# Performance work log

Measured on AMD Instinct MI355X. Metric: run time of the kernel, lower is better.

Reference implementation:

```python
import jax, jax.numpy as jnp
import numpy as np
import math

N, E, G = 16000, 128000, 64
D, H, O, L, HID = 64, 4, 64, 5, 128
EPS = 1e-5

def _ln(x, g, b):
    mu = x.mean(-1, keepdims=True)
    var = ((x - mu) ** 2).mean(-1, keepdims=True)
    return (x - mu) / jnp.sqrt(var + EPS) * g + b

def _softplus_b64(x):
    # torch nn.Softplus(beta=64, threshold=64): x if 64*x > 64 else log1p(exp(64*x))/64
    z = jnp.minimum(x * 64.0, 64.0)
    return jnp.where(x * 64.0 > 64.0, x, jnp.log1p(jnp.exp(z)) / 64.0)

def setup_inputs() -> dict:
    key = jax.random.key(0)
    ks = jax.random.split(key, 32)
    s = 0.05
    d = {
        'x': jax.random.normal(ks[0], (N, 4), jnp.float32),
        'edge_attr': jax.random.normal(ks[1], (E, 9), jnp.float32),
        'edge_index': jax.random.randint(ks[2], (2, E), 0, N),
        'batch': jnp.sort(jax.random.randint(ks[3], (N,), 0, G)),
        'W_atom': jax.random.normal(ks[4], (4, D)) * s, 'b_atom': jnp.zeros((D,)),
        'We1': jax.random.normal(ks[5], (9, D)) * s, 'be1': jnp.zeros((D,)),
        'We2': jax.random.normal(ks[6], (D, D)) * s, 'be2': jnp.zeros((D,)),
        'Wq': jax.random.normal(ks[7], (L, D, H * O)) * s, 'bq': jnp.zeros((L, H * O)),
        'Wk': jax.random.normal(ks[8], (L, D, H * O)) * s, 'bk': jnp.zeros((L, H * O)),
        'Wv': jax.random.normal(ks[9], (L, D, H * O)) * s, 'bv': jnp.zeros((L, H * O)),
        'Wedge': jax.random.normal(ks[10], (L, D, H * O)) * s, 'bedge': jnp.zeros((L, H * O)),
        'Wfea': jax.random.normal(ks[11], (L, D, O)) * s, 'bfea': jnp.zeros((L, O)),
        'Wcat': jax.random.normal(ks[12], (L, H * O, O)) * s, 'bcat': jnp.zeros((L, O)),
        'Wupd': jax.random.normal(ks[13], (L, 3 * O, 3 * O)) * s, 'bupd': jnp.zeros((L, 3 * O)),
        'Wmsg': jax.random.normal(ks[14], (L, 3 * O, O)) * s, 'bmsg': jnp.zeros((L, O)),
        'g_msg': jnp.ones((L, O)), 'be_msg': jnp.zeros((L, O)),
        'g_ln': jnp.ones((L, 3 * O)), 'be_ln': jnp.zeros((L, 3 * O)),
        'g_bn': jnp.ones((L, O)), 'be_bn': jnp.zeros((L, O)),
        'Wfc': jax.random.normal(ks[15], (D, HID)) * s, 'bfc': jnp.zeros((HID,)),
        'Wout': jax.random.normal(ks[16], (HID, 1)) * s, 'bout': jnp.zeros((1,)),
    }
    return d

def _forward(x, edge_attr, W_atom, b_atom, We1, be1, We2, be2, Wq, bq, Wk, bk, Wv, bv,
             Wedge, bedge, Wfea, bfea, Wcat, bcat, Wupd, bupd, Wmsg, bmsg,
             g_msg, be_msg, g_ln, be_ln, g_bn, be_bn, Wfc, bfc, Wout, bout,
             edge_index, batch):
    src, dst = edge_index[0], edge_index[1]  # x_j = src, x_i = dst (flow source_to_target)
    h = x @ W_atom + b_atom  # [N, D]
    e = _softplus_b64(edge_attr @ We1 + be1) @ We2 + be2  # [E, D]
    scale = 1.0 / math.sqrt(3.0 * O)
    for l in range(L):
        Q = (h @ Wq[l] + bq[l]).reshape(N, H, O)
        K = (h @ Wk[l] + bk[l]).reshape(N, H, O)
        V = (h @ Wv[l] + bv[l]).reshape(N, H, O)
        Eh = (e @ Wedge[l] + bedge[l]).reshape(E, H, O)
        Qi = Q[dst]
        q_ij = jnp.concatenate([Qi, Qi, Qi], axis=-1)                 # [E, H, 3O]
        k_ij = jnp.concatenate([K[dst], K[src], Eh], axis=-1)
        v_ij = jnp.concatenate([V[dst], V[src], Eh], axis=-1)
        alpha = q_ij * k_ij * scale
        gate = jax.nn.sigmoid(_ln(alpha, g_ln[l], be_ln[l]))
        m = gate * (v_ij @ Wupd[l] + bupd[l])
        m = _ln(m @ Wmsg[l] + bmsg[l], g_msg[l], be_msg[l])           # [E, H, O]
        agg = jax.ops.segment_sum(m, dst, num_segments=N).reshape(N, H * O)
        out = agg @ Wcat[l] + bcat[l]
        mu = out.mean(0)
        var = ((out - mu) ** 2).mean(0)  # biased var, BN training mode
        out = (out - mu) / jnp.sqrt(var + EPS) * g_bn[l] + be_bn[l]
        h = jax.nn.silu(out) + (h @ Wfea[l] + bfea[l])
    ones = jnp.ones((N,), h.dtype)
    cnt = jax.ops.segment_sum(ones, batch, num_segments=G)
    pooled = jax.ops.segment_sum(h, batch, num_segments=G) / jnp.maximum(cnt, 1.0)[:, None]
    z = jax.nn.silu(pooled @ Wfc + bfc)
    return z @ Wout + bout  # [G, 1]

def reference(x, edge_attr, edge_index, batch, W_atom, b_atom, We1, be1, We2, be2,
              Wq, bq, Wk, bk, Wv, bv, Wedge, bedge, Wfea, bfea, Wcat, bcat,
              Wupd, bupd, Wmsg, bmsg, g_msg, be_msg, g_ln, be_ln, g_bn, be_bn,
              Wfc, bfc, Wout, bout):
    return _forward(x, edge_attr, W_atom, b_atom, We1, be1, We2, be2, Wq, bq, Wk, bk,
                    Wv, bv, Wedge, bedge, Wfea, bfea, Wcat, bcat, Wupd, bupd,
                    Wmsg, bmsg, g_msg, be_msg, g_ln, be_ln, g_bn, be_bn,
                    Wfc, bfc, Wout, bout, edge_index, batch)
```

## Files before the change

kernel.cpp:

```cpp
#include <hip/hip_runtime.h>
#include <hip/hip_bf16.h>
#include <math.h>

#define N_NODES 16000
#define N_EDGES 128000
#define N_GRAPH 64
#define NL 5
#define EPSV 1e-5f
#define SCALE 0.07216878364870323f

#define PC 2048
#define ECOLS 1024
#define TILE 16
#define SCR 260

typedef __hip_bfloat16 bf16;
typedef __attribute__((ext_vector_type(8))) short short8;
typedef __attribute__((ext_vector_type(4))) short s4v;
typedef __attribute__((ext_vector_type(4))) float f32x4;
union S8U { short8 v; s4v h[2]; };

__device__ __forceinline__ ushort f2b(float x) {
    union { float f; uint u; } v; v.f = x;
    uint r = v.u + 0x7fffu + ((v.u >> 16) & 1u);
    return (ushort)(r >> 16);
}
__device__ __forceinline__ float b2fu(ushort u) { union { uint u; float f; } v; v.u = (uint)u << 16; return v.f; }

__global__ void pack_w(const float* __restrict__ Wq, const float* __restrict__ Wk,
                       const float* __restrict__ Wv, const float* __restrict__ Wupd,
                       const float* __restrict__ Wedge,
                       short* __restrict__ Wnp, short* __restrict__ Wep) {
    int idx = blockIdx.x * 256 + threadIdx.x;
    int total = NL * 64 * (PC + ECOLS);
    if (idx >= total) return;
    int c = idx % (PC + ECOLS);
    int k = (idx / (PC + ECOLS)) % 64;
    int l = idx / (64 * (PC + ECOLS));
    if (c < PC) {
        float v = 0.f;
        if (c < 256) v = Wq[(l*64 + k)*256 + c];
        else if (c < 512) v = Wk[(l*64 + k)*256 + (c - 256)];
        else if (c < 1280) {
            int cc = c - 512, hd = cc / 192, p = cc % 192;
            float s = 0.f;
            for (int q = 0; q < 64; ++q)
                s += Wv[(l*64 + k)*256 + hd*64 + q] * Wupd[(l*192 + q)*192 + p];
            v = s;
        } else {
            int cc = c - 1280, hd = cc / 192, p = cc % 192;
            float s = 0.f;
            for (int q = 0; q < 64; ++q)
                s += Wv[(l*64 + k)*256 + hd*64 + q] * Wupd[(l*192 + 64 + q)*192 + p];
            v = s;
        }
        int t = c >> 4, s = k >> 5, lane = (c & 15) | (((k & 31) >> 3) << 4), jj = k & 7;
        size_t fo = ((size_t)(t*2 + s)*64 + lane)*8 + jj;
        ushort hi = f2b(v);
        ushort lo = f2b(v - b2fu(hi));
        Wnp[(size_t)l*2*64*PC + fo] = (short)hi;
        Wnp[(size_t)l*2*64*PC + (size_t)64*PC + fo] = (short)lo;
    } else {
        int ce = c - PC;
        float v;
        if (ce < 256) v = Wedge[(l*64 + k)*256 + ce];
        else {
            int cc = ce - 256, hd = cc / 192, p = cc % 192;
            float s = 0.f;
            for (int q = 0; q < 64; ++q)
                s += Wedge[(l*64 + k)*256 + hd*64 + q] * Wupd[(l*192 + 128 + q)*192 + p];
            v = s;
        }
        int t = ce >> 4, s = k >> 5, lane = (ce & 15) | (((k & 31) >> 3) << 4), jj = k & 7;
        size_t fo = ((size_t)(t*2 + s)*64 + lane)*8 + jj;
        ushort hi = f2b(v);
        ushort lo = f2b(v - b2fu(hi));
        Wep[(size_t)l*2*64*ECOLS + fo] = (short)hi;
        Wep[(size_t)l*2*64*ECOLS + (size_t)64*ECOLS + fo] = (short)lo;
    }
}

__global__ void pack_wmsg(const float* __restrict__ Wmsg, short* __restrict__ Wmf) {
    int idx = blockIdx.x * 256 + threadIdx.x;
    if (idx >= NL*192*64) return;
    int col = idx & 63, k = (idx >> 6) % 192, l = idx / (192*64);
    float v = Wmsg[(size_t)(l*192 + k)*64 + col];
    int t = col >> 4, s = k >> 5, lane = (col & 15) | (((k & 31) >> 3) << 4), j = k & 7;
    Wmf[(size_t)l*12288 + ((size_t)((t*6 + s)*64) + lane)*8 + j] = (short)f2b(v);
}

__global__ void pack_b(const float* __restrict__ bq, const float* __restrict__ bk,
                       const float* __restrict__ bv, const float* __restrict__ Wupd,
                       const float* __restrict__ bupd, const float* __restrict__ bedge,
                       float* __restrict__ bnp, float* __restrict__ bep) {
    int idx = blockIdx.x * 256 + threadIdx.x;
    int total = NL * (PC + ECOLS);
    if (idx >= total) return;
    int c = idx % (PC + ECOLS);
    int l = idx / (PC + ECOLS);
    if (c < PC) {
        float v = 0.f;
        if (c < 256) v = bq[l*256 + c];
        else if (c < 512) v = bk[l*256 + c - 256];
        else if (c < 1280) {
            int cc = c - 512, hd = cc / 192, p = cc % 192;
            float s = 0.f;
            for (int k = 0; k < 64; ++k) s += bv[l*256 + hd*64 + k] * Wupd[(l*192 + k)*192 + p];
            v = s;
        } else {
            int cc = c - 1280, hd = cc / 192, p = cc % 192;
            float s = 0.f;
            for (int k = 0; k < 64; ++k) s += bv[l*256 + hd*64 + k] * Wupd[(l*192 + 64 + k)*192 + p];
            v = s;
        }
        bnp[l*PC + c] = v;
    } else {
        int ce = c - PC;
        float v;
        if (ce < 256) v = bedge[l*256 + ce];
        else {
            int cc = ce - 256, hd = cc / 192, p = cc % 192;
            float s = bupd[l*192 + p];
            for (int k = 0; k < 64; ++k) s += bedge[l*256 + hd*64 + k] * Wupd[(l*192 + 128 + k)*192 + p];
            v = s;
        }
        bep[l*ECOLS + ce] = v;
    }
}

__global__ void hist_k(const int* __restrict__ ei, int* __restrict__ hist) {
    int e = blockIdx.x * 256 + threadIdx.x;
    if (e < N_EDGES) atomicAdd(&hist[ei[N_EDGES + e]], 1);
}

__global__ void scan_k(const int* __restrict__ hist, int* __restrict__ binCur) {
    __shared__ int sBuf[256];
    __shared__ int sCarry;
    int tid = threadIdx.x;
    if (tid == 0) sCarry = 0;
    __syncthreads();
    for (int base = 0; base < N_NODES; base += 256) {
        int v = (base + tid < N_NODES) ? hist[base + tid] : 0;
        sBuf[tid] = v; __syncthreads();
        #pragma unroll
        for (int ofs = 1; ofs < 256; ofs <<= 1) {
            int t = (tid >= ofs) ? sBuf[tid - ofs] : 0;
            __syncthreads();
            sBuf[tid] += t;
            __syncthreads();
        }
        if (base + tid < N_NODES) binCur[base + tid] = sCarry + sBuf[tid] - v;
        __syncthreads();
        if (tid == 0) sCarry += sBuf[255];
        __syncthreads();
    }
}

__global__ void scatter_k(const int* __restrict__ ei, int* __restrict__ binCur,
                          int* __restrict__ perm, int* __restrict__ srcs, int* __restrict__ dsts) {
    int e = blockIdx.x * 256 + threadIdx.x;
    if (e < N_EDGES) {
        int d = ei[N_EDGES + e];
        int pos = atomicAdd(&binCur[d], 1);
        perm[pos] = e;
        srcs[pos] = ei[e];
        dsts[pos] = d;
    }
}

__global__ void init_h(const float* __restrict__ x, const float* __restrict__ W_atom,
                       const float* __restrict__ b_atom, float* __restrict__ h) {
    int idx = blockIdx.x * 256 + threadIdx.x;
    int d = idx & 63, n = idx >> 6;
    float s = b_atom[d];
    #pragma unroll
    for (int j = 0; j < 4; ++j) s += x[n*4 + j] * W_atom[j*64 + d];
    h[idx] = s;
}

__global__ void init_e(const float* __restrict__ ea, const float* __restrict__ We1,
                       const float* __restrict__ be1, const float* __restrict__ We2,
                       const float* __restrict__ be2, float* __restrict__ ef) {
    __shared__ float sT[4][64];
    int tid = threadIdx.x, d = tid & 63, sub = tid >> 6;
    int e = blockIdx.x * 4 + sub;
    float s = be1[d];
    #pragma unroll
    for (int j = 0; j < 9; ++j) s += ea[e*9 + j] * We1[j*64 + d];
    float x64 = s * 64.f;
    float sp = (x64 > 64.f) ? s : log1pf(__expf(fminf(x64, 64.f))) * (1.f/64.f);
    sT[sub][d] = sp;
    float acc = be2[d];
    #pragma unroll
    for (int k = 0; k < 64; ++k) acc += sT[sub][k] * We2[k*64 + d];
    ef[(size_t)e*64 + d] = acc;
}

#define CPAD 260
__global__ __launch_bounds__(256, 8) void proj_mfma(
    const float* __restrict__ A, const short* __restrict__ Whi, const short* __restrict__ Wlo,
    const float* __restrict__ bias, ushort* __restrict__ out, int M) {
    __shared__ short aHi[2*64*8];
    __shared__ short aLo[2*64*8];
    __shared__ ushort cTile[16*CPAD];
    int tid = threadIdx.x;
    int row0 = blockIdx.y * 16;
    int col0 = blockIdx.x * 256;
    {
        int r = tid >> 4, k0 = (tid & 15) * 4;
        const float4 v = *(const float4*)(A + (size_t)(row0 + r)*64 + k0);
        int s = k0 >> 5, lane = r | (((k0 & 31) >> 3) << 4), j0 = k0 & 7;
        ushort4 hb, lb;
        hb.x = f2b(v.x); lb.x = f2b(v.x - b2fu(hb.x));
        hb.y = f2b(v.y); lb.y = f2b(v.y - b2fu(hb.y));
        hb.z = f2b(v.z); lb.z = f2b(v.z - b2fu(hb.z));
        hb.w = f2b(v.w); lb.w = f2b(v.w - b2fu(hb.w));
        *(ushort4*)&aHi[(s*64 + lane)*8 + j0] = hb;
        *(ushort4*)&aLo[(s*64 + lane)*8 + j0] = lb;
    }
    __syncthreads();
    int w = tid >> 6, lane = tid & 63;
    short8 a0h = *(const short8*)&aHi[(0*64 + lane)*8];
    short8 a1h = *(const short8*)&aHi[(1*64 + lane)*8];
    short8 a0l = *(const short8*)&aLo[(0*64 + lane)*8];
    short8 a1l = *(const short8*)&aLo[(1*64 + lane)*8];
    int cl = lane & 15, rg = lane >> 4;
    #pragma unroll
    for (int nt = 0; nt < 4; ++nt) {
        int t = (col0 >> 4) + w*4 + nt;
        const short* bph = Whi + ((size_t)(t*2)*64 + lane)*8;
        const short* bpl = Wlo + ((size_t)(t*2)*64 + lane)*8;
        short8 b0h = *(const short8*)bph;
        short8 b1h = *(const short8*)(bph + 64*8);
        short8 b0l = *(const short8*)bpl;
        short8 b1l = *(const short8*)(bpl + 64*8);
        f32x4 acc = {0.f, 0.f, 0.f, 0.f};
        acc = __builtin_amdgcn_mfma_f32_16x16x32_bf16(a0h, b0h, acc, 0, 0, 0);
        acc = __builtin_amdgcn_mfma_f32_16x16x32_bf16(a1h, b1h, acc, 0, 0, 0);
        acc = __builtin_amdgcn_mfma_f32_16x16x32_bf16(a0l, b0h, acc, 0, 0, 0);
        acc = __builtin_amdgcn_mfma_f32_16x16x32_bf16(a1l, b1h, acc, 0, 0, 0);
        acc = __builtin_amdgcn_mfma_f32_16x16x32_bf16(a0h, b0l, acc, 0, 0, 0);
        acc = __builtin_amdgcn_mfma_f32_16x16x32_bf16(a1h, b1l, acc, 0, 0, 0);
        int ccol = w*64 + nt*16 + cl;
        float bv = bias[col0 + ccol];
        #pragma unroll
        for (int r = 0; r < 4; ++r)
            cTile[(rg*4 + r)*CPAD + ccol] = f2b(acc[r] + bv);
    }
    __syncthreads();
    {
        int r = tid >> 4, cs = (tid & 15) * 16;
        ushort* dst = out + (size_t)(row0 + r)*M + col0 + cs;
        const ushort* srcp = &cTile[r*CPAD + cs];
        #pragma unroll
        for (int q = 0; q < 4; ++q)
            *(ushort4*)(dst + q*4) = *(const ushort4*)(srcp + q*4);
    }
}

__global__ __launch_bounds__(256) void hf_proj(const float* __restrict__ h,
                                               const float* __restrict__ Wfea,
                                               const float* __restrict__ bfea,
                                               float* __restrict__ HF) {
    __shared__ float sW[64*64];
    __shared__ __align__(16) float sA[4][64];
    int tid = threadIdx.x;
    for (int i = tid; i < 4096; i += 256) sW[i] = Wfea[i];
    int c = tid & 63, no = tid >> 6;
    int n0 = blockIdx.x * 4;
    sA[no][c] = h[(size_t)(n0 + no)*64 + c];
    __syncthreads();
    float acc = bfea[c];
    #pragma unroll
    for (int k4 = 0; k4 < 16; ++k4) {
        float4 av = *(const float4*)&sA[no][k4*4];
        acc += av.x*sW[(k4*4+0)*64+c] + av.y*sW[(k4*4+1)*64+c]
             + av.z*sW[(k4*4+2)*64+c] + av.w*sW[(k4*4+3)*64+c];
    }
    HF[(size_t)(n0 + no)*64 + c] = acc;
}

__global__ __launch_bounds__(256, 4) void edge_fused(
    const bf16* __restrict__ P, const float* __restrict__ ef,
    const short* __restrict__ Wef, const float* __restrict__ bef,
    const int* __restrict__ perm, const int* __restrict__ srcs, const int* __restrict__ dsts,
    const short* __restrict__ Wmf, const float* __restrict__ bmsg,
    const float* __restrict__ g_ln, const float* __restrict__ be_ln,
    const float* __restrict__ g_msg, const float* __restrict__ be_msg,
    float* __restrict__ agg) {
    __shared__ short aHi[2*64*8];
    __shared__ short aLo[2*64*8];
    __shared__ __align__(16) ushort scr[4][TILE][SCR];
    int tid = threadIdx.x, lane = tid & 63, hd = tid >> 6;
    int e0 = blockIdx.x * TILE;
    {
        int r = tid >> 4, k0 = (tid & 15) * 4;
        int ep = perm[e0 + r];
        const float4 v = *(const float4*)(ef + (size_t)ep*64 + k0);
        int s = k0 >> 5, alane = r | (((k0 & 31) >> 3) << 4), j0 = k0 & 7;
        ushort4 hb, lb;
        hb.x = f2b(v.x); lb.x = f2b(v.x - b2fu(hb.x));
        hb.y = f2b(v.y); lb.y = f2b(v.y - b2fu(hb.y));
        hb.z = f2b(v.z); lb.z = f2b(v.z - b2fu(hb.z));
        hb.w = f2b(v.w); lb.w = f2b(v.w - b2fu(hb.w));
        *(ushort4*)&aHi[(s*64 + alane)*8 + j0] = hb;
        *(ushort4*)&aLo[(s*64 + alane)*8 + j0] = lb;
    }
    __syncthreads();
    int cl = lane & 15, rg = lane >> 4;
    {
        short8 a0h = *(const short8*)&aHi[(0*64 + lane)*8];
        short8 a1h = *(const short8*)&aHi[(1*64 + lane)*8];
        short8 a0l = *(const short8*)&aLo[(0*64 + lane)*8];
        short8 a1l = *(const short8*)&aLo[(1*64 + lane)*8];
        #pragma unroll
        for (int tt = 0; tt < 16; ++tt) {
            int tg = (tt < 4) ? (hd*4 + tt) : (16 + hd*12 + (tt - 4));
            const short* bph = Wef + ((size_t)(tg*2)*64 + lane)*8;
            const short* bpl = bph + (size_t)64*ECOLS;
            short8 b0h = *(const short8*)bph;
            short8 b1h = *(const short8*)(bph + 512);
            short8 b0l = *(const short8*)bpl;
            short8 b1l = *(const short8*)(bpl + 512);
            float bv = bef[tg*16 + cl];
            f32x4 acc = {bv, bv, bv, bv};
            acc = __builtin_amdgcn_mfma_f32_16x16x32_bf16(a0h, b0h, acc, 0, 0, 0);
            acc = __builtin_amdgcn_mfma_f32_16x16x32_bf16(a1h, b1h, acc, 0, 0, 0);
            acc = __builtin_amdgcn_mfma_f32_16x16x32_bf16(a0l, b0h, acc, 0, 0, 0);
            acc = __builtin_amdgcn_mfma_f32_16x16x32_bf16(a1l, b1h, acc, 0, 0, 0);
            acc = __builtin_amdgcn_mfma_f32_16x16x32_bf16(a0h, b0l, acc, 0, 0, 0);
            acc = __builtin_amdgcn_mfma_f32_16x16x32_bf16(a1h, b1l, acc, 0, 0, 0);
            int wcol = (tt < 4) ? (tt*16 + cl) : (64 + (tt - 4)*16 + cl);
            #pragma unroll
            for (int r = 0; r < 4; ++r)
                scr[hd][rg*4 + r][wcol] = f2b(acc[r]);
        }
    }
    float gl0 = g_ln[lane], gl1 = g_ln[64 + lane], gl2 = g_ln[128 + lane];
    float bl0 = be_ln[lane], bl1 = be_ln[64 + lane], bl2 = be_ln[128 + lane];
    #pragma unroll 2
    for (int it = 0; it < TILE; ++it) {
        int src = srcs[e0 + it], dst = dsts[e0 + it];
        const bf16* Pd = P + (size_t)dst * PC;
        const bf16* Ps = P + (size_t)src * PC;
        float q  = __bfloat162float(Pd[hd*64 + lane]);
        float kd = __bfloat162float(Pd[256 + hd*64 + lane]);
        float ks = __bfloat162float(Ps[256 + hd*64 + lane]);
        float eh = b2fu(scr[hd][it][lane]);
        float a0 = q*kd*SCALE, a1 = q*ks*SCALE, a2 = q*eh*SCALE;
        float s = a0 + a1 + a2, ss = a0*a0 + a1*a1 + a2*a2;
        #pragma unroll
        for (int m = 1; m < 64; m <<= 1) { s += __shfl_xor(s, m); ss += __shfl_xor(ss, m); }
        float mu = s * (1.f/192.f);
        float var = ss * (1.f/192.f) - mu*mu;
        float rstd = rsqrtf(var + EPSV);
        float g0 = 1.f/(1.f + __expf(-((a0 - mu)*rstd*gl0 + bl0)));
        float g1 = 1.f/(1.f + __expf(-((a1 - mu)*rstd*gl1 + bl1)));
        float g2 = 1.f/(1.f + __expf(-((a2 - mu)*rstd*gl2 + bl2)));
        float vu0 = __bfloat162float(Pd[512 + hd*192 + lane])
                  + __bfloat162float(Ps[1280 + hd*192 + lane])
                  + b2fu(scr[hd][it][64 + lane]);
        float vu1 = __bfloat162float(Pd[512 + hd*192 + 64 + lane])
                  + __bfloat162float(Ps[1280 + hd*192 + 64 + lane])
                  + b2fu(scr[hd][it][128 + lane]);
        float vu2 = __bfloat162float(Pd[512 + hd*192 + 128 + lane])
                  + __bfloat162float(Ps[1280 + hd*192 + 128 + lane])
                  + b2fu(scr[hd][it][192 + lane]);
        scr[hd][it][64 + lane]  = f2b(g0*vu0);
        scr[hd][it][128 + lane] = f2b(g1*vu1);
        scr[hd][it][192 + lane] = f2b(g2*vu2);
    }
    float bmsv[4], gmv[4], bmv[4];
    #pragma unroll
    for (int t = 0; t < 4; ++t) {
        bmsv[t] = bmsg[t*16 + cl];
        gmv[t]  = g_msg[t*16 + cl];
        bmv[t]  = be_msg[t*16 + cl];
    }
    int dstr[4];
    #pragma unroll
    for (int r = 0; r < 4; ++r) dstr[r] = dsts[e0 + rg*4 + r];
    f32x4 acc[4];
    #pragma unroll
    for (int t = 0; t < 4; ++t) acc[t] = (f32x4){bmsv[t], bmsv[t], bmsv[t], bmsv[t]};
    #pragma unroll
    for (int s = 0; s < 6; ++s) {
        S8U a;
        const ushort* ap = &scr[hd][cl][64 + s*32 + rg*8];
        a.h[0] = *(const s4v*)ap;
        a.h[1] = *(const s4v*)(ap + 4);
        #pragma unroll
        for (int t = 0; t < 4; ++t) {
            short8 b = *(const short8*)&Wmf[((size_t)((t*6 + s)*64) + lane)*8];
            acc[t] = __builtin_amdgcn_mfma_f32_16x16x32_bf16(a.v, b, acc[t], 0, 0, 0);
        }
    }
    float nv[4][4];
    #pragma unroll
    for (int r = 0; r < 4; ++r) {
        float s1 = acc[0][r] + acc[1][r] + acc[2][r] + acc[3][r];
        float s2 = acc[0][r]*acc[0][r] + acc[1][r]*acc[1][r]
                 + acc[2][r]*acc[2][r] + acc[3][r]*acc[3][r];
        #pragma unroll
        for (int m = 1; m < 16; m <<= 1) { s1 += __shfl_xor(s1, m); s2 += __shfl_xor(s2, m); }
        float mu = s1 * (1.f/64.f);
        float var = s2 * (1.f/64.f) - mu*mu;
        float rstd = rsqrtf(var + EPSV);
        #pragma unroll
        for (int t = 0; t < 4; ++t) nv[t][r] = (acc[t][r] - mu)*rstd*gmv[t] + bmv[t];
    }
    int cur = dstr[0];
    float r0 = nv[0][0], r1 = nv[1][0], r2 = nv[2][0], r3 = nv[3][0];
    #pragma unroll
    for (int r = 1; r < 4; ++r) {
        if (dstr[r] == cur) {
            r0 += nv[0][r]; r1 += nv[1][r]; r2 += nv[2][r]; r3 += nv[3][r];
        } else {
            float* base = &agg[(size_t)cur*256 + hd*64];
            atomicAdd(base + 0*16 + cl, r0);
            atomicAdd(base + 1*16 + cl, r1);
            atomicAdd(base + 2*16 + cl, r2);
            atomicAdd(base + 3*16 + cl, r3);
            cur = dstr[r];
            r0 = nv[0][r]; r1 = nv[1][r]; r2 = nv[2][r]; r3 = nv[3][r];
        }
    }
    {
        float* base = &agg[(size_t)cur*256 + hd*64];
        atomicAdd(base + 0*16 + cl, r0);
        atomicAdd(base + 1*16 + cl, r1);
        atomicAdd(base + 2*16 + cl, r2);
        atomicAdd(base + 3*16 + cl, r3);
    }
}

__global__ __launch_bounds__(256, 2) void agg_out(
    const float* __restrict__ agg, const float* __restrict__ Wcat, const float* __restrict__ bcat,
    float* __restrict__ out, float* __restrict__ bnsum, float* __restrict__ bnss) {
    __shared__ float sW[256 * 64];
    __shared__ __align__(16) float sA[4][256];
    __shared__ float sR[4][64];
    int tid = threadIdx.x;
    for (int i = tid; i < 256*64; i += 256) sW[i] = Wcat[i];
    int c = tid & 63, no = tid >> 6;
    float bc = bcat[c];
    float psum = 0.f, psq = 0.f;
    __syncthreads();
    int nbase = blockIdx.x * 64;
    for (int it = 0; it < 16; ++it) {
        for (int i = tid; i < 1024; i += 256)
            sA[i >> 8][i & 255] = agg[(size_t)(nbase + it*4 + (i >> 8))*256 + (i & 255)];
        __syncthreads();
        float acc = bc;
        #pragma unroll
        for (int k4 = 0; k4 < 64; ++k4) {
            float4 av = *(const float4*)&sA[no][k4*4];
            acc += av.x*sW[(k4*4+0)*64 + c] + av.y*sW[(k4*4+1)*64 + c]
                 + av.z*sW[(k4*4+2)*64 + c] + av.w*sW[(k4*4+3)*64 + c];
        }
        out[(size_t)(nbase + it*4 + no)*64 + c] = acc;
        psum += acc; psq += acc*acc;
        __syncthreads();
    }
    sR[no][c] = psum; __syncthreads();
    if (no == 0) atomicAdd(&bnsum[c], sR[0][c] + sR[1][c] + sR[2][c] + sR[3][c]);
    __syncthreads();
    sR[no][c] = psq; __syncthreads();
    if (no == 0) atomicAdd(&bnss[c], sR[0][c] + sR[1][c] + sR[2][c] + sR[3][c]);
}

__global__ void bn_silu(const float* __restrict__ out, const float* __restrict__ HF,
                        const float* __restrict__ bnsum, const float* __restrict__ bnss,
                        const float* __restrict__ g_bn, const float* __restrict__ be_bn,
                        float* __restrict__ h) {
    int idx = blockIdx.x * 256 + threadIdx.x;
    int c = idx & 63;
    float mu = bnsum[c] * (1.f/N_NODES);
    float var = bnss[c] * (1.f/N_NODES) - mu*mu;
    float rstd = rsqrtf(var + EPSV);
    float v = (out[idx] - mu)*rstd*g_bn[c] + be_bn[c];
    float sv = v / (1.f + __expf(-v));
    h[idx] = sv + HF[idx];
}

__device__ __forceinline__ int lbound(const int* __restrict__ a, int n, int v) {
    int lo = 0, hi = n;
    while (lo < hi) { int m = (lo + hi) >> 1; if (a[m] < v) lo = m + 1; else hi = m; }
    return lo;
}

__global__ __launch_bounds__(256) void pool_head(
    const float* __restrict__ h, const int* __restrict__ batch,
    const float* __restrict__ Wfc, const float* __restrict__ bfc,
    const float* __restrict__ Wout, const float* __restrict__ bout,
    float* __restrict__ d_out) {
    __shared__ float sPart[4][64];
    __shared__ float sP[64];
    __shared__ float red[128];
    int g = blockIdx.x, tid = threadIdx.x;
    int lo = lbound(batch, N_NODES, g);
    int hi = lbound(batch, N_NODES, g + 1);
    int c = tid & 63, rg = tid >> 6;
    float s = 0.f;
    for (int n = lo + rg; n < hi; n += 4) s += h[(size_t)n*64 + c];
    sPart[rg][c] = s;
    __syncthreads();
    if (tid < 64)
        sP[tid] = (sPart[0][tid] + sPart[1][tid] + sPart[2][tid] + sPart[3][tid])
                  * (1.f / fmaxf((float)(hi - lo), 1.f));
    __syncthreads();
    if (tid < 128) {
        float acc = bfc[tid];
        #pragma unroll
        for (int k = 0; k < 64; ++k) acc += sP[k] * Wfc[k*128 + tid];
        float z = acc / (1.f + __expf(-acc));
        red[tid] = z * Wout[tid];
    }
    __syncthreads();
    for (int s1 = 64; s1 > 0; s1 >>= 1) {
        if (tid < s1 && tid + s1 < 128) red[tid] += red[tid + s1];
        __syncthreads();
    }
    if (tid == 0) d_out[g] = red[0] + bout[0];
}

extern "C" void kernel_launch(void* const* d_in, const int* in_sizes, int n_in,
                              void* d_out, int out_size, void* d_ws, size_t ws_size,
                              hipStream_t stream) {
    const float* x        = (const float*)d_in[0];
    const float* edge_attr= (const float*)d_in[1];
    const int*   ei       = (const int*)  d_in[2];
    const int*   batch    = (const int*)  d_in[3];
    const float* W_atom=(const float*)d_in[4];  const float* b_atom=(const float*)d_in[5];
    const float* We1  =(const float*)d_in[6];   const float* be1  =(const float*)d_in[7];
    const float* We2  =(const float*)d_in[8];   const float* be2  =(const float*)d_in[9];
    const float* Wq   =(const float*)d_in[10];  const float* bq   =(const float*)d_in[11];
    const float* Wk   =(const float*)d_in[12];  const float* bk   =(const float*)d_in[13];
    const float* Wv   =(const float*)d_in[14];  const float* bv   =(const float*)d_in[15];
    const float* Wedge=(const float*)d_in[16];  const float* bedge=(const float*)d_in[17];
    const float* Wfea =(const float*)d_in[18];  const float* bfea =(const float*)d_in[19];
    const float* Wcat =(const float*)d_in[20];  const float* bcat =(const float*)d_in[21];
    const float* Wupd =(const float*)d_in[22];  const float* bupd =(const float*)d_in[23];
    const float* Wmsg =(const float*)d_in[24];  const float* bmsg =(const float*)d_in[25];
    const float* g_msg=(const float*)d_in[26];  const float* be_msg=(const float*)d_in[27];
    const float* g_ln =(const float*)d_in[28];  const float* be_ln=(const float*)d_in[29];
    const float* g_bn =(const float*)d_in[30];  const float* be_bn=(const float*)d_in[31];
    const float* Wfc  =(const float*)d_in[32];  const float* bfc  =(const float*)d_in[33];
    const float* Wout =(const float*)d_in[34];  const float* bout =(const float*)d_in[35];

    char* ws = (char*)d_ws;
    size_t off = 0;
    auto alloc = [&](size_t bytes) {
        void* p = ws + off;
        off += (bytes + 255) & ~(size_t)255;
        return p;
    };
    short* Wnp  = (short*)alloc((size_t)NL*2*64*PC*2);
    float* bnp  = (float*)alloc((size_t)NL*PC*4);
    short* Wep  = (short*)alloc((size_t)NL*2*64*ECOLS*2);
    float* bep  = (float*)alloc((size_t)NL*ECOLS*4);
    short* Wmf  = (short*)alloc((size_t)NL*12288*2);
    float* h    = (float*)alloc((size_t)N_NODES*64*4);
    float* ef   = (float*)alloc((size_t)N_EDGES*64*4);
    bf16*  P    = (bf16*) alloc((size_t)N_NODES*PC*2);
    float* HF   = (float*)alloc((size_t)N_NODES*64*4);
    float* agg  = (float*)alloc((size_t)N_NODES*256*4);
    float* outb = (float*)alloc((size_t)N_NODES*64*4);
    float* bnsum= (float*)alloc(64*4);
    float* bnss = (float*)alloc(64*4);
    int* histB  = (int*)alloc((size_t)N_NODES*4);
    int* binCur = (int*)alloc((size_t)N_NODES*4);
    int* perm   = (int*)alloc((size_t)N_EDGES*4);
    int* srcs   = (int*)alloc((size_t)N_EDGES*4);
    int* dsts   = (int*)alloc((size_t)N_EDGES*4);
    if (off > ws_size) return;

    {
        int total = NL*64*(PC+ECOLS);
        pack_w<<<(total+255)/256, 256, 0, stream>>>(Wq, Wk, Wv, Wupd, Wedge, Wnp, Wep);
        int tb = NL*(PC+ECOLS);
        pack_b<<<(tb+255)/256, 256, 0, stream>>>(bq, bk, bv, Wupd, bupd, bedge, bnp, bep);
        pack_wmsg<<<(NL*192*64+255)/256, 256, 0, stream>>>(Wmsg, Wmf);
    }
    hipMemsetAsync(histB, 0, (size_t)N_NODES*4, stream);
    hist_k<<<(N_EDGES+255)/256, 256, 0, stream>>>(ei, histB);
    scan_k<<<1, 256, 0, stream>>>(histB, binCur);
    scatter_k<<<(N_EDGES+255)/256, 256, 0, stream>>>(ei, binCur, perm, srcs, dsts);

    init_h<<<(N_NODES*64)/256, 256, 0, stream>>>(x, W_atom, b_atom, h);
    init_e<<<N_EDGES/4, 256, 0, stream>>>(edge_attr, We1, be1, We2, be2, ef);

    for (int l = 0; l < NL; ++l) {
        const short* Wh = Wnp + (size_t)l*2*64*PC;
        proj_mfma<<<dim3(PC/256, N_NODES/16), 256, 0, stream>>>(
            h, Wh, Wh + (size_t)64*PC, bnp + l*PC, (ushort*)P, PC);
        hf_proj<<<N_NODES/4, 256, 0, stream>>>(h, Wfea + (size_t)l*64*64, bfea + l*64, HF);
        hipMemsetAsync(agg, 0, (size_t)N_NODES*256*4, stream);
        hipMemsetAsync(bnsum, 0, 64*4, stream);
        hipMemsetAsync(bnss, 0, 64*4, stream);
        edge_fused<<<N_EDGES/TILE, 256, 0, stream>>>(
            P, ef, Wep + (size_t)l*2*64*ECOLS, bep + l*ECOLS, perm, srcs, dsts,
            Wmf + (size_t)l*12288, bmsg + l*64,
            g_ln + l*192, be_ln + l*192, g_msg + l*64, be_msg + l*64, agg);
        agg_out<<<N_NODES/64, 256, 0, stream>>>(agg, Wcat + (size_t)l*256*64, bcat + l*64,
                                                outb, bnsum, bnss);
        bn_silu<<<(N_NODES*64)/256, 256, 0, stream>>>(outb, HF, bnsum, bnss,
                                                      g_bn + l*64, be_bn + l*64, h);
    }
    pool_head<<<N_GRAPH, 256, 0, stream>>>(h, batch, Wfc, bfc, Wout, bout, (float*)d_out);
}
```

Baseline: 1.712 ms.

## Interleave node projection columns per channel for vectorized gathers in edge kernel

Reorders the packed node-projection columns so each head/channel's q, k and the six value-update terms sit contiguously in 8 bf16s. The edge kernel can then fetch them with one 16-byte and one 8-byte load per endpoint instead of many scattered 2-byte gathers. It also builds the edge-feature MFMA operands directly in registers, dropping the LDS staging and a barrier, and uses a fast reciprocal for the sigmoid gates. As an accuracy fix, Wmsg gets a hi/lo bf16 split, which doubles that GEMM's MFMA count.

```diff
diff --git a/kernel.cpp b/kernel.cpp
--- a/kernel.cpp
+++ b/kernel.cpp
@@ -9,7 +9,7 @@
 #define EPSV 1e-5f
 #define SCALE 0.07216878364870323f
 
-#define PC 2048
+#define PCK 2048
 #define ECOLS 1024
 #define TILE 16
 #define SCR 260
@@ -26,29 +26,32 @@
     return (ushort)(r >> 16);
 }
 __device__ __forceinline__ float b2fu(ushort u) { union { uint u; float f; } v; v.u = (uint)u << 16; return v.f; }
+__device__ __forceinline__ float b2f_lo32(uint u) { union { uint u; float f; } v; v.u = u << 16; return v.f; }
+__device__ __forceinline__ float b2f_hi32(uint u) { union { uint u; float f; } v; v.u = u & 0xffff0000u; return v.f; }
 
 __global__ void pack_w(const float* __restrict__ Wq, const float* __restrict__ Wk,
                        const float* __restrict__ Wv, const float* __restrict__ Wupd,
                        const float* __restrict__ Wedge,
                        short* __restrict__ Wnp, short* __restrict__ Wep) {
     int idx = blockIdx.x * 256 + threadIdx.x;
-    int total = NL * 64 * (PC + ECOLS);
+    int total = NL * 64 * (PCK + ECOLS);
     if (idx >= total) return;
-    int c = idx % (PC + ECOLS);
-    int k = (idx / (PC + ECOLS)) % 64;
-    int l = idx / (64 * (PC + ECOLS));
-    if (c < PC) {
-        float v = 0.f;
-        if (c < 256) v = Wq[(l*64 + k)*256 + c];
-        else if (c < 512) v = Wk[(l*64 + k)*256 + (c - 256)];
-        else if (c < 1280) {
-            int cc = c - 512, hd = cc / 192, p = cc % 192;
+    int c = idx % (PCK + ECOLS);
+    int k = (idx / (PCK + ECOLS)) % 64;
+    int l = idx / (64 * (PCK + ECOLS));
+    if (c < PCK) {
+        int hd = c >> 9, ch = (c >> 3) & 63, j = c & 7;
+        float v;
+        if (j == 0) v = Wq[(l*64 + k)*256 + hd*64 + ch];
+        else if (j == 4) v = Wk[(l*64 + k)*256 + hd*64 + ch];
+        else if (j < 4) {
+            int p = (j - 1)*64 + ch;
             float s = 0.f;
             for (int q = 0; q < 64; ++q)
                 s += Wv[(l*64 + k)*256 + hd*64 + q] * Wupd[(l*192 + q)*192 + p];
             v = s;
         } else {
-            int cc = c - 1280, hd = cc / 192, p = cc % 192;
+            int p = (j - 5)*64 + ch;
             float s = 0.f;
             for (int q = 0; q < 64; ++q)
                 s += Wv[(l*64 + k)*256 + hd*64 + q] * Wupd[(l*192 + 64 + q)*192 + p];
@@ -58,10 +61,10 @@
         size_t fo = ((size_t)(t*2 + s)*64 + lane)*8 + jj;
         ushort hi = f2b(v);
         ushort lo = f2b(v - b2fu(hi));
-        Wnp[(size_t)l*2*64*PC + fo] = (short)hi;
-        Wnp[(size_t)l*2*64*PC + (size_t)64*PC + fo] = (short)lo;
+        Wnp[(size_t)l*2*64*PCK + fo] = (short)hi;
+        Wnp[(size_t)l*2*64*PCK + (size_t)64*PCK + fo] = (short)lo;
     } else {
-        int ce = c - PC;
+        int ce = c - PCK;
         float v;
         if (ce < 256) v = Wedge[(l*64 + k)*256 + ce];
         else {
@@ -86,7 +89,11 @@
     int col = idx & 63, k = (idx >> 6) % 192, l = idx / (192*64);
     float v = Wmsg[(size_t)(l*192 + k)*64 + col];
     int t = col >> 4, s = k >> 5, lane = (col & 15) | (((k & 31) >> 3) << 4), j = k & 7;
-    Wmf[(size_t)l*12288 + ((size_t)((t*6 + s)*64) + lane)*8 + j] = (short)f2b(v);
+    size_t fo = ((size_t)((t*6 + s)*64) + lane)*8 + j;
+    ushort hi = f2b(v);
+    ushort lo = f2b(v - b2fu(hi));
+    Wmf[(size_t)l*2*12288 + fo] = (short)hi;
+    Wmf[(size_t)l*2*12288 + 12288 + fo] = (short)lo;
 }
 
 __global__ void pack_b(const float* __restrict__ bq, const float* __restrict__ bk,
@@ -94,28 +101,29 @@
                        const float* __restrict__ bupd, const float* __restrict__ bedge,
                        float* __restrict__ bnp, float* __restrict__ bep) {
     int idx = blockIdx.x * 256 + threadIdx.x;
-    int total = NL * (PC + ECOLS);
+    int total = NL * (PCK + ECOLS);
     if (idx >= total) return;
-    int c = idx % (PC + ECOLS);
-    int l = idx / (PC + ECOLS);
-    if (c < PC) {
-        float v = 0.f;
-        if (c < 256) v = bq[l*256 + c];
-        else if (c < 512) v = bk[l*256 + c - 256];
-        else if (c < 1280) {
-            int cc = c - 512, hd = cc / 192, p = cc % 192;
+    int c = idx % (PCK + ECOLS);
+    int l = idx / (PCK + ECOLS);
+    if (c < PCK) {
+        int hd = c >> 9, ch = (c >> 3) & 63, j = c & 7;
+        float v;
+        if (j == 0) v = bq[l*256 + hd*64 + ch];
+        else if (j == 4) v = bk[l*256 + hd*64 + ch];
+        else if (j < 4) {
+            int p = (j - 1)*64 + ch;
             float s = 0.f;
             for (int k = 0; k < 64; ++k) s += bv[l*256 + hd*64 + k] * Wupd[(l*192 + k)*192 + p];
             v = s;
         } else {
-            int cc = c - 1280, hd = cc / 192, p = cc % 192;
+            int p = (j - 5)*64 + ch;
             float s = 0.f;
             for (int k = 0; k < 64; ++k) s += bv[l*256 + hd*64 + k] * Wupd[(l*192 + 64 + k)*192 + p];
             v = s;
         }
-        bnp[l*PC + c] = v;
+        bnp[l*PCK + c] = v;
     } else {
-        int ce = c - PC;
+        int ce = c - PCK;
         float v;
         if (ce < 256) v = bedge[l*256 + ce];
         else {
@@ -281,38 +289,46 @@
 }
 
 __global__ __launch_bounds__(256, 4) void edge_fused(
-    const bf16* __restrict__ P, const float* __restrict__ ef,
+    const ushort* __restrict__ Pu, const float* __restrict__ ef,
     const short* __restrict__ Wef, const float* __restrict__ bef,
     const int* __restrict__ perm, const int* __restrict__ srcs, const int* __restrict__ dsts,
     const short* __restrict__ Wmf, const float* __restrict__ bmsg,
     const float* __restrict__ g_ln, const float* __restrict__ be_ln,
     const float* __restrict__ g_msg, const float* __restrict__ be_msg,
     float* __restrict__ agg) {
-    __shared__ short aHi[2*64*8];
-    __shared__ short aLo[2*64*8];
     __shared__ __align__(16) ushort scr[4][TILE][SCR];
     int tid = threadIdx.x, lane = tid & 63, hd = tid >> 6;
     int e0 = blockIdx.x * TILE;
-    {
-        int r = tid >> 4, k0 = (tid & 15) * 4;
-        int ep = perm[e0 + r];
-        const float4 v = *(const float4*)(ef + (size_t)ep*64 + k0);
-        int s = k0 >> 5, alane = r | (((k0 & 31) >> 3) << 4), j0 = k0 & 7;
-        ushort4 hb, lb;
-        hb.x = f2b(v.x); lb.x = f2b(v.x - b2fu(hb.x));
-        hb.y = f2b(v.y); lb.y = f2b(v.y - b2fu(hb.y));
-        hb.z = f2b(v.z); lb.z = f2b(v.z - b2fu(hb.z));
-        hb.w = f2b(v.w); lb.w = f2b(v.w - b2fu(hb.w));
-        *(ushort4*)&aHi[(s*64 + alane)*8 + j0] = hb;
-        *(ushort4*)&aLo[(s*64 + alane)*8 + j0] = lb;
-    }
-    __syncthreads();
     int cl = lane & 15, rg = lane >> 4;
     {
-        short8 a0h = *(const short8*)&aHi[(0*64 + lane)*8];
-        short8 a1h = *(const short8*)&aHi[(1*64 + lane)*8];
-        short8 a0l = *(const short8*)&aLo[(0*64 + lane)*8];
-        short8 a1l = *(const short8*)&aLo[(1*64 + lane)*8];
+        int ep = perm[e0 + cl];
+        const float* ar = ef + (size_t)ep*64 + (rg << 3);
+        float4 v0a = *(const float4*)ar,        v0b = *(const float4*)(ar + 4);
+        float4 v1a = *(const float4*)(ar + 32), v1b = *(const float4*)(ar + 36);
+        S8U a0h, a0l, a1h, a1l;
+        {
+            ushort4 h0, l0, h1, l1;
+            h0.x = f2b(v0a.x); l0.x = f2b(v0a.x - b2fu(h0.x));
+            h0.y = f2b(v0a.y); l0.y = f2b(v0a.y - b2fu(h0.y));
+            h0.z = f2b(v0a.z); l0.z = f2b(v0a.z - b2fu(h0.z));
+            h0.w = f2b(v0a.w); l0.w = f2b(v0a.w - b2fu(h0.w));
+            h1.x = f2b(v0b.x); l1.x = f2b(v0b.x - b2fu(h1.x));
+            h1.y = f2b(v0b.y); l1.y = f2b(v0b.y - b2fu(h1.y));
+            h1.z = f2b(v0b.z); l1.z = f2b(v0b.z - b2fu(h1.z));
+            h1.w = f2b(v0b.w); l1.w = f2b(v0b.w - b2fu(h1.w));
+            a0h.h[0] = *(s4v*)&h0; a0h.h[1] = *(s4v*)&h1;
+            a0l.h[0] = *(s4v*)&l0; a0l.h[1] = *(s4v*)&l1;
+            h0.x = f2b(v1a.x); l0.x = f2b(v1a.x - b2fu(h0.x));
+            h0.y = f2b(v1a.y); l0.y = f2b(v1a.y - b2fu(h0.y));
+            h0.z = f2b(v1a.z); l0.z = f2b(v1a.z - b2fu(h0.z));
+            h0.w = f2b(v1a.w); l0.w = f2b(v1a.w - b2fu(h0.w));
+            h1.x = f2b(v1b.x); l1.x = f2b(v1b.x - b2fu(h1.x));
+            h1.y = f2b(v1b.y); l1.y = f2b(v1b.y - b2fu(h1.y));
+            h1.z = f2b(v1b.z); l1.z = f2b(v1b.z - b2fu(h1.z));
+            h1.w = f2b(v1b.w); l1.w = f2b(v1b.w - b2fu(h1.w));
+            a1h.h[0] = *(s4v*)&h0; a1h.h[1] = *(s4v*)&h1;
+            a1l.h[0] = *(s4v*)&l0; a1l.h[1] = *(s4v*)&l1;
+        }
         #pragma unroll
         for (int tt = 0; tt < 16; ++tt) {
             int tg = (tt < 4) ? (hd*4 + tt) : (16 + hd*12 + (tt - 4));
@@ -324,12 +340,12 @@
             short8 b1l = *(const short8*)(bpl + 512);
             float bv = bef[tg*16 + cl];
             f32x4 acc = {bv, bv, bv, bv};
-            acc = __builtin_amdgcn_mfma_f32_16x16x32_bf16(a0h, b0h, acc, 0, 0, 0);
-            acc = __builtin_amdgcn_mfma_f32_16x16x32_bf16(a1h, b1h, acc, 0, 0, 0);
-            acc = __builtin_amdgcn_mfma_f32_16x16x32_bf16(a0l, b0h, acc, 0, 0, 0);
-            acc = __builtin_amdgcn_mfma_f32_16x16x32_bf16(a1l, b1h, acc, 0, 0, 0);
-            acc = __builtin_amdgcn_mfma_f32_16x16x32_bf16(a0h, b0l, acc, 0, 0, 0);
-            acc = __builtin_amdgcn_mfma_f32_16x16x32_bf16(a1h, b1l, acc, 0, 0, 0);
+            acc = __builtin_amdgcn_mfma_f32_16x16x32_bf16(a0h.v, b0h, acc, 0, 0, 0);
+            acc = __builtin_amdgcn_mfma_f32_16x16x32_bf16(a1h.v, b1h, acc, 0, 0, 0);
+            acc = __builtin_amdgcn_mfma_f32_16x16x32_bf16(a0l.v, b0h, acc, 0, 0, 0);
+            acc = __builtin_amdgcn_mfma_f32_16x16x32_bf16(a1l.v, b1h, acc, 0, 0, 0);
+            acc = __builtin_amdgcn_mfma_f32_16x16x32_bf16(a0h.v, b0l, acc, 0, 0, 0);
+            acc = __builtin_amdgcn_mfma_f32_16x16x32_bf16(a1h.v, b1l, acc, 0, 0, 0);
             int wcol = (tt < 4) ? (tt*16 + cl) : (64 + (tt - 4)*16 + cl);
             #pragma unroll
             for (int r = 0; r < 4; ++r)
@@ -338,14 +354,16 @@
     }
     float gl0 = g_ln[lane], gl1 = g_ln[64 + lane], gl2 = g_ln[128 + lane];
     float bl0 = be_ln[lane], bl1 = be_ln[64 + lane], bl2 = be_ln[128 + lane];
-    #pragma unroll 2
+    #pragma unroll 4
     for (int it = 0; it < TILE; ++it) {
         int src = srcs[e0 + it], dst = dsts[e0 + it];
-        const bf16* Pd = P + (size_t)dst * PC;
-        const bf16* Ps = P + (size_t)src * PC;
-        float q  = __bfloat162float(Pd[hd*64 + lane]);
-        float kd = __bfloat162float(Pd[256 + hd*64 + lane]);
-        float ks = __bfloat162float(Ps[256 + hd*64 + lane]);
+        const uint4 D = *(const uint4*)(Pu + (size_t)dst*PCK + hd*512 + (lane << 3));
+        const uint2 S = *(const uint2*)(Pu + (size_t)src*PCK + hd*512 + (lane << 3) + 4);
+        float q   = b2f_lo32(D.x), vd0 = b2f_hi32(D.x);
+        float vd1 = b2f_lo32(D.y), vd2 = b2f_hi32(D.y);
+        float kd  = b2f_lo32(D.z);
+        float ks  = b2f_lo32(S.x), vs0 = b2f_hi32(S.x);
+        float vs1 = b2f_lo32(S.y), vs2 = b2f_hi32(S.y);
         float eh = b2fu(scr[hd][it][lane]);
         float a0 = q*kd*SCALE, a1 = q*ks*SCALE, a2 = q*eh*SCALE;
         float s = a0 + a1 + a2, ss = a0*a0 + a1*a1 + a2*a2;
@@ -354,18 +372,12 @@
         float mu = s * (1.f/192.f);
         float var = ss * (1.f/192.f) - mu*mu;
         float rstd = rsqrtf(var + EPSV);
-        float g0 = 1.f/(1.f + __expf(-((a0 - mu)*rstd*gl0 + bl0)));
-        float g1 = 1.f/(1.f + __expf(-((a1 - mu)*rstd*gl1 + bl1)));
-        float g2 = 1.f/(1.f + __expf(-((a2 - mu)*rstd*gl2 + bl2)));
-        float vu0 = __bfloat162float(Pd[512 + hd*192 + lane])
-                  + __bfloat162float(Ps[1280 + hd*192 + lane])
-                  + b2fu(scr[hd][it][64 + lane]);
-        float vu1 = __bfloat162float(Pd[512 + hd*192 + 64 + lane])
-                  + __bfloat162float(Ps[1280 + hd*192 + 64 + lane])
-                  + b2fu(scr[hd][it][128 + lane]);
-        float vu2 = __bfloat162float(Pd[512 + hd*192 + 128 + lane])
-                  + __bfloat162float(Ps[1280 + hd*192 + 128 + lane])
-                  + b2fu(scr[hd][it][192 + lane]);
+        float g0 = __builtin_amdgcn_rcpf(1.f + __expf(-((a0 - mu)*rstd*gl0 + bl0)));
+        float g1 = __builtin_amdgcn_rcpf(1.f + __expf(-((a1 - mu)*rstd*gl1 + bl1)));
+        float g2 = __builtin_amdgcn_rcpf(1.f + __expf(-((a2 - mu)*rstd*gl2 + bl2)));
+        float vu0 = vd0 + vs0 + b2fu(scr[hd][it][64 + lane]);
+        float vu1 = vd1 + vs1 + b2fu(scr[hd][it][128 + lane]);
+        float vu2 = vd2 + vs2 + b2fu(scr[hd][it][192 + lane]);
         scr[hd][it][64 + lane]  = f2b(g0*vu0);
         scr[hd][it][128 + lane] = f2b(g1*vu1);
         scr[hd][it][192 + lane] = f2b(g2*vu2);
@@ -391,8 +403,11 @@
         a.h[1] = *(const s4v*)(ap + 4);
         #pragma unroll
         for (int t = 0; t < 4; ++t) {
-            short8 b = *(const short8*)&Wmf[((size_t)((t*6 + s)*64) + lane)*8];
-            acc[t] = __builtin_amdgcn_mfma_f32_16x16x32_bf16(a.v, b, acc[t], 0, 0, 0);
+            const short* bp = &Wmf[((size_t)((t*6 + s)*64) + lane)*8];
+            short8 bh = *(const short8*)bp;
+            short8 bl = *(const short8*)(bp + 12288);
+            acc[t] = __builtin_amdgcn_mfma_f32_16x16x32_bf16(a.v, bh, acc[t], 0, 0, 0);
+            acc[t] = __builtin_amdgcn_mfma_f32_16x16x32_bf16(a.v, bl, acc[t], 0, 0, 0);
         }
     }
     float nv[4][4];
@@ -555,14 +570,14 @@
         off += (bytes + 255) & ~(size_t)255;
         return p;
     };
-    short* Wnp  = (short*)alloc((size_t)NL*2*64*PC*2);
-    float* bnp  = (float*)alloc((size_t)NL*PC*4);
+    short* Wnp  = (short*)alloc((size_t)NL*2*64*PCK*2);
+    float* bnp  = (float*)alloc((size_t)NL*PCK*4);
     short* Wep  = (short*)alloc((size_t)NL*2*64*ECOLS*2);
     float* bep  = (float*)alloc((size_t)NL*ECOLS*4);
-    short* Wmf  = (short*)alloc((size_t)NL*12288*2);
+    short* Wmf  = (short*)alloc((size_t)NL*2*12288*2);
     float* h    = (float*)alloc((size_t)N_NODES*64*4);
     float* ef   = (float*)alloc((size_t)N_EDGES*64*4);
-    bf16*  P    = (bf16*) alloc((size_t)N_NODES*PC*2);
+    ushort* P   = (ushort*)alloc((size_t)N_NODES*PCK*2);
     float* HF   = (float*)alloc((size_t)N_NODES*64*4);
     float* agg  = (float*)alloc((size_t)N_NODES*256*4);
     float* outb = (float*)alloc((size_t)N_NODES*64*4);
@@ -576,9 +591,9 @@
     if (off > ws_size) return;
 
     {
-        int total = NL*64*(PC+ECOLS);
+        int total = NL*64*(PCK+ECOLS);
         pack_w<<<(total+255)/256, 256, 0, stream>>>(Wq, Wk, Wv, Wupd, Wedge, Wnp, Wep);
-        int tb = NL*(PC+ECOLS);
+        int tb = NL*(PCK+ECOLS);
         pack_b<<<(tb+255)/256, 256, 0, stream>>>(bq, bk, bv, Wupd, bupd, bedge, bnp, bep);
         pack_wmsg<<<(NL*192*64+255)/256, 256, 0, stream>>>(Wmsg, Wmf);
     }
@@ -591,16 +606,16 @@
     init_e<<<N_EDGES/4, 256, 0, stream>>>(edge_attr, We1, be1, We2, be2, ef);
 
     for (int l = 0; l < NL; ++l) {
-        const short* Wh = Wnp + (size_t)l*2*64*PC;
-        proj_mfma<<<dim3(PC/256, N_NODES/16), 256, 0, stream>>>(
-            h, Wh, Wh + (size_t)64*PC, bnp + l*PC, (ushort*)P, PC);
+        const short* Wh = Wnp + (size_t)l*2*64*PCK;
+        proj_mfma<<<dim3(PCK/256, N_NODES/16), 256, 0, stream>>>(
+            h, Wh, Wh + (size_t)64*PCK, bnp + l*PCK, P, PCK);
         hf_proj<<<N_NODES/4, 256, 0, stream>>>(h, Wfea + (size_t)l*64*64, bfea + l*64, HF);
         hipMemsetAsync(agg, 0, (size_t)N_NODES*256*4, stream);
         hipMemsetAsync(bnsum, 0, 64*4, stream);
         hipMemsetAsync(bnss, 0, 64*4, stream);
         edge_fused<<<N_EDGES/TILE, 256, 0, stream>>>(
             P, ef, Wep + (size_t)l*2*64*ECOLS, bep + l*ECOLS, perm, srcs, dsts,
-            Wmf + (size_t)l*12288, bmsg + l*64,
+            Wmf + (size_t)l*2*12288, bmsg + l*64,
             g_ln + l*192, be_ln + l*192, g_msg + l*64, be_msg + l*64, agg);
         agg_out<<<N_NODES/64, 256, 0, stream>>>(agg, Wcat + (size_t)l*256*64, bcat + l*64,
                                                 outb, bnsum, bnss);
```

Result: slower. 1.883 ms (+10.0%).
